# Kernel tuning notes

Hardware: AMD Instinct MI355X
Metric: run time of the kernel (lower is better)

Reference implementation:

```python
import jax, jax.numpy as jnp
import numpy as np

VOCAB = 780
HIDDEN = 256
DEPTH = 6
N_NODES = 65536
N_MESS = 131072
MAX_NEI = 5
N_TREES = 2048


def setup_inputs() -> dict:
    key = jax.random.key(0)
    ks = jax.random.split(key, 16)
    s = 0.05  # weight scale to avoid gate saturation
    return {
        "fnode": jax.random.randint(ks[0], (N_NODES,), 0, VOCAB),
        "fmess": jax.random.randint(ks[1], (N_MESS,), 0, N_NODES),
        "node_graph": jax.random.randint(ks[2], (N_NODES, MAX_NEI), 0, N_MESS),
        "mess_graph": jax.random.randint(ks[3], (N_MESS, MAX_NEI), 0, N_MESS),
        "scope_ids": jnp.sort(jax.random.randint(ks[4], (N_NODES,), 0, N_TREES)),
        "emb": jax.random.normal(ks[5], (VOCAB, HIDDEN), jnp.float32) * s,
        "Wz_w": jax.random.normal(ks[6], (2 * HIDDEN, HIDDEN), jnp.float32) * s,
        "Wz_b": jax.random.normal(ks[7], (HIDDEN,), jnp.float32) * s,
        "Wr_w": jax.random.normal(ks[8], (HIDDEN, HIDDEN), jnp.float32) * s,
        "Ur_w": jax.random.normal(ks[9], (HIDDEN, HIDDEN), jnp.float32) * s,
        "Ur_b": jax.random.normal(ks[10], (HIDDEN,), jnp.float32) * s,
        "Wh_w": jax.random.normal(ks[11], (2 * HIDDEN, HIDDEN), jnp.float32) * s,
        "Wh_b": jax.random.normal(ks[12], (HIDDEN,), jnp.float32) * s,
        "out_w": jax.random.normal(ks[13], (2 * HIDDEN, HIDDEN), jnp.float32) * s,
        "out_b": jax.random.normal(ks[14], (HIDDEN,), jnp.float32) * s,
    }


def reference(fnode, fmess, node_graph, mess_graph, scope_ids,
              emb, Wz_w, Wz_b, Wr_w, Ur_w, Ur_b, Wh_w, Wh_b, out_w, out_b):
    x_node = emb[fnode]            # [N, H] embedding lookup
    x = x_node[fmess]              # [M, H] source-node feature per message
    M = mess_graph.shape[0]
    mask = jnp.ones((M, 1), x.dtype).at[0].set(0.0)  # message 0 is padding
    r1 = x @ Wr_w                  # W_r(x), constant across depth (no bias)

    def gru_step(h, _):
        h_nei = h[mess_graph]                                  # [M, K, H] gather
        sum_h = h_nei.sum(axis=1)                              # [M, H]
        z = jax.nn.sigmoid(jnp.concatenate([x, sum_h], 1) @ Wz_w + Wz_b)
        r = jax.nn.sigmoid(r1[:, None, :] + h_nei @ Ur_w + Ur_b)  # [M, K, H]
        sum_gh = (r * h_nei).sum(axis=1)
        pre_h = jnp.tanh(jnp.concatenate([x, sum_gh], 1) @ Wh_w + Wh_b)
        h_new = ((1.0 - z) * sum_h + z * pre_h) * mask
        return h_new, None

    h0 = jnp.zeros((M, HIDDEN), x.dtype)
    h, _ = jax.lax.scan(gru_step, h0, None, length=DEPTH)

    mess_nei = h[node_graph].sum(axis=1)                       # [N, H]
    node_vec = jax.nn.relu(jnp.concatenate([x_node, mess_nei], 1) @ out_w + out_b)

    # per-tree mean over contiguous scopes (segment mean)
    sums = jax.ops.segment_sum(node_vec, scope_ids, num_segments=N_TREES)
    counts = jax.ops.segment_sum(jnp.ones((node_vec.shape[0],), node_vec.dtype),
                                 scope_ids, num_segments=N_TREES)
    return sums / jnp.maximum(counts, 1.0)[:, None]
```

## Files before the change

kernel.cpp:

```cpp
#include <hip/hip_runtime.h>


#define HD 256
#define NNODES 65536
#define NMESS 131072
#define NVOCAB 780
#define NTREES 2048
#define MAXNEI 5
#define BM 128
#define BMF 32
#define LDF 264

typedef short bfrag __attribute__((ext_vector_type(8)));
typedef short s16x8 __attribute__((ext_vector_type(8)));
typedef float f32x4v __attribute__((ext_vector_type(4)));
typedef unsigned short ush;

__device__ __forceinline__ float bf2f(ush u) {
    union { unsigned int u; float f; } v; v.u = ((unsigned int)u) << 16; return v.f;
}
__device__ __forceinline__ ush f2bf_fast(float f) {
    union { float f; unsigned int u; } v; v.f = f;
    return (ush)((v.u + 0x8000u) >> 16);
}
__device__ __forceinline__ unsigned int pack2bf(float hi, float lo) {
    union { float f; unsigned int u; } a, b; a.f = hi; b.f = lo;
    return __builtin_amdgcn_perm(a.u + 0x8000u, b.u + 0x8000u, 0x07060302u);
}
__device__ __forceinline__ float sigm(float x) {
    return __builtin_amdgcn_rcpf(1.f + __expf(-x));
}
__device__ __forceinline__ float tanh_fast(float x) {
    return 1.f - 2.f * __builtin_amdgcn_rcpf(__expf(2.f * x) + 1.f);
}
__device__ __forceinline__ void async16(const ush* g, ush* l) {
    __builtin_amdgcn_global_load_lds(
        (const __attribute__((address_space(1))) unsigned int*)(g),
        (__attribute__((address_space(3))) unsigned int*)(l), 16, 0, 0);
}

__global__ __launch_bounds__(256) void prep_tables_sk(
    const float* __restrict__ emb,
    const float* __restrict__ Wz_w, const float* __restrict__ Wz_b,
    const float* __restrict__ Wr_w, const float* __restrict__ Ur_b,
    const float* __restrict__ Wh_w, const float* __restrict__ Wh_b,
    const float* __restrict__ out_w, const float* __restrict__ out_b,
    float* __restrict__ embR, float* __restrict__ embZ,
    float* __restrict__ embH, float* __restrict__ embO)
{
    __shared__ __align__(16) float e[4][64];
    int t = threadIdx.x;
    int b0 = blockIdx.x * 4;
    int k0 = blockIdx.y * 64;
    e[t >> 6][t & 63] = emb[(b0 + (t >> 6)) * HD + k0 + (t & 63)];
    __syncthreads();
    float aR[4] = {0,0,0,0}, aZ[4] = {0,0,0,0}, aH[4] = {0,0,0,0}, aO[4] = {0,0,0,0};
    for (int kk = 0; kk < 64; kk++) {
        int k = k0 + kk;
        float wr = Wr_w[k * HD + t];
        float wz = Wz_w[k * HD + t];
        float wh = Wh_w[k * HD + t];
        float wo = out_w[k * HD + t];
        #pragma unroll
        for (int r = 0; r < 4; r++) {
            float ev = e[r][kk];
            aR[r] += ev * wr; aZ[r] += ev * wz; aH[r] += ev * wh; aO[r] += ev * wo;
        }
    }
    if (blockIdx.y == 0) {
        float br = Ur_b[t], bz = Wz_b[t], bh = Wh_b[t], bo = out_b[t];
        #pragma unroll
        for (int r = 0; r < 4; r++) { aR[r] += br; aZ[r] += bz; aH[r] += bh; aO[r] += bo; }
    }
    #pragma unroll
    for (int r = 0; r < 4; r++) {
        atomicAdd(&embR[(b0 + r) * HD + t], aR[r]);
        atomicAdd(&embZ[(b0 + r) * HD + t], aZ[r]);
        atomicAdd(&embH[(b0 + r) * HD + t], aH[r]);
        atomicAdd(&embO[(b0 + r) * HD + t], aO[r]);
    }
}

__global__ __launch_bounds__(256) void h1fill(
    const float* __restrict__ embZ, const float* __restrict__ embH,
    ush* __restrict__ h1tab)
{
    int i = blockIdx.x * HD + threadIdx.x;
    h1tab[i] = f2bf_fast(sigm(embZ[i]) * tanh_fast(embH[i]));
}

__global__ __launch_bounds__(256) void h1u_sk(
    const ush* __restrict__ h1tab, const float* __restrict__ Ur_w,
    float* __restrict__ embU)
{
    __shared__ __align__(16) float e[4][64];
    int t = threadIdx.x;
    int b0 = blockIdx.x * 4;
    int k0 = blockIdx.y * 64;
    e[t >> 6][t & 63] = bf2f(h1tab[(b0 + (t >> 6)) * HD + k0 + (t & 63)]);
    __syncthreads();
    float aU[4] = {0,0,0,0};
    for (int kk = 0; kk < 64; kk++) {
        float w = Ur_w[(k0 + kk) * HD + t];
        #pragma unroll
        for (int r = 0; r < 4; r++) aU[r] += e[r][kk] * w;
    }
    #pragma unroll
    for (int r = 0; r < 4; r++) atomicAdd(&embU[(b0 + r) * HD + t], aU[r]);
}

__global__ __launch_bounds__(256) void prep_wt(
    const float* __restrict__ Ur_w, const float* __restrict__ Wz_w,
    const float* __restrict__ Wh_w, const float* __restrict__ out_w,
    ush* __restrict__ UrT, ush* __restrict__ Wo2T,
    ush* __restrict__ Wz_p, ush* __restrict__ Wh_p)
{
    int idx = blockIdx.x * 256 + threadIdx.x;
    int n = idx >> 8, k = idx & 255;
    UrT[idx]  = f2bf_fast(Ur_w[k * HD + n]);
    Wo2T[idx] = f2bf_fast(out_w[(HD + k) * HD + n]);
    int paddr = ((((n >> 4) * 8 + (k >> 5)) * 64 + ((k >> 3) & 3) * 16 + (n & 15)) << 3) + (k & 7);
    Wz_p[paddr] = f2bf_fast(Wz_w[(HD + k) * HD + n]);
    Wh_p[paddr] = f2bf_fast(Wh_w[(HD + k) * HD + n]);
}

__global__ __launch_bounds__(256) void prep_vmess(
    const int* __restrict__ fnode, const int* __restrict__ fmess,
    int* __restrict__ v_mess)
{
    int m = blockIdx.x * 256 + threadIdx.x;
    v_mess[m] = fnode[fmess[m]];
}

__global__ __launch_bounds__(256) void fill_h1(
    const ush* __restrict__ h1tab, const float* __restrict__ embU,
    const int* __restrict__ v_mess,
    ush* __restrict__ h, ush* __restrict__ hU)
{
    int t = blockIdx.x * 256 + threadIdx.x;
    int m = t >> 5;
    int c = (t & 31) * 8;
    int v = v_mess[m];
    s16x8 o = *(const s16x8*)&h1tab[v * HD + c];
    float4 u0 = *(const float4*)&embU[v * HD + c];
    float4 u1 = *(const float4*)&embU[v * HD + c + 4];
    uint4 up;
    up.x = pack2bf(u0.y, u0.x); up.y = pack2bf(u0.w, u0.z);
    up.z = pack2bf(u1.y, u1.x); up.w = pack2bf(u1.w, u1.z);
    if (m == 0) { o = (s16x8){0,0,0,0,0,0,0,0}; up.x = up.y = up.z = up.w = 0; }
    *(s16x8*)&h[(size_t)m * HD + c] = o;
    *(uint4*)&hU[(size_t)m * HD + c] = up;
}

template<int MODE>
__global__ __launch_bounds__(512) void gemm_tile(
    const ush* __restrict__ A, const ush* __restrict__ Bt,
    void* __restrict__ C,
    const float* __restrict__ etab, const int* __restrict__ vids)
{
    __shared__ __align__(16) ush As[BM * 64];
    __shared__ __align__(16) ush Bs[HD * 64];
    int tid = threadIdx.x;
    int wave = tid >> 6, lane = tid & 63;
    int wm = wave >> 2, wn = wave & 3;
    int quad = lane >> 4, l16 = lane & 15;
    int row0 = blockIdx.x * BM;

    const ush* aG[2]; ush* aL[2];
    const ush* bG[4]; ush* bL[4];
    #pragma unroll
    for (int u = 0; u < 2; u++) {
        int cch = wave * 2 + u;
        int s = cch * 64 + lane;
        int r = s >> 3, p = s & 7, q = p ^ (r & 7);
        aG[u] = A + (size_t)(row0 + r) * HD + q * 8;
        aL[u] = &As[cch * 512];
    }
    #pragma unroll
    for (int u = 0; u < 4; u++) {
        int cch = wave * 4 + u;
        int s = cch * 64 + lane;
        int r = s >> 3, p = s & 7, q = p ^ (r & 7);
        bG[u] = Bt + (size_t)r * HD + q * 8;
        bL[u] = &Bs[cch * 512];
    }

    f32x4v acc[4][4] = {};

    for (int k0 = 0; k0 < HD; k0 += 64) {
        #pragma unroll
        for (int u = 0; u < 2; u++) async16(aG[u] + k0, aL[u]);
        #pragma unroll
        for (int u = 0; u < 4; u++) async16(bG[u] + k0, bL[u]);
        __syncthreads();
        #pragma unroll
        for (int ks = 0; ks < 64; ks += 32) {
            bfrag af[4], bff[4];
            #pragma unroll
            for (int i = 0; i < 4; i++) {
                int r = wm * 64 + i * 16 + l16;
                int q = (ks >> 3) + quad, p = q ^ (r & 7);
                af[i] = *(const bfrag*)&As[r * 64 + p * 8];
            }
            #pragma unroll
            for (int j = 0; j < 4; j++) {
                int r = wn * 64 + j * 16 + l16;
                int q = (ks >> 3) + quad, p = q ^ (r & 7);
                bff[j] = *(const bfrag*)&Bs[r * 64 + p * 8];
            }
            #pragma unroll
            for (int i = 0; i < 4; i++)
                #pragma unroll
                for (int j = 0; j < 4; j++)
                    acc[i][j] = __builtin_amdgcn_mfma_f32_16x16x32_bf16(af[i], bff[j], acc[i][j], 0, 0, 0);
        }
        __syncthreads();
    }
    #pragma unroll
    for (int i = 0; i < 4; i++) {
        #pragma unroll
        for (int j = 0; j < 4; j++) {
            int Cc = wn * 64 + j * 16 + l16;
            #pragma unroll
            for (int r = 0; r < 4; r++) {
                int Rr = row0 + wm * 64 + i * 16 + quad * 4 + r;
                float v = acc[i][j][r];
                if (MODE == 0) {
                    ((ush*)C)[(size_t)Rr * HD + Cc] = f2bf_fast(v);
                } else {
                    float o = v + etab[vids[Rr] * HD + Cc];
                    ((float*)C)[(size_t)Rr * HD + Cc] = fmaxf(o, 0.f);
                }
            }
        }
    }
}

__global__ __launch_bounds__(256, 4) void fused_step(
    const ush* __restrict__ h, const ush* __restrict__ hU,
    const int* __restrict__ mg, const int* __restrict__ v_mess,
    const float* __restrict__ embR, const float* __restrict__ embZ,
    const float* __restrict__ embH,
    const ush* __restrict__ Wz_p, const ush* __restrict__ Wh_p,
    ush* __restrict__ h_next)
{
    __shared__ __align__(16) ush sh[BMF * LDF];
    __shared__ __align__(16) ush sg[BMF * LDF];
    int tid = threadIdx.x;
    int wv = tid >> 6, lane = tid & 63;
    int quad = lane >> 4, l16 = lane & 15;
    int m0 = blockIdx.x * BMF;

    #pragma unroll 2
    for (int it = 0; it < 4; it++) {
        int g = it * 256 + tid;
        int ml = g >> 5;
        int c = (g & 31) * 8;
        int m = m0 + ml;
        int v = v_mess[m];
        float rb[8];
        *(float4*)&rb[0] = *(const float4*)&embR[v * HD + c];
        *(float4*)&rb[4] = *(const float4*)&embR[v * HD + c + 4];
        float ah[8] = {0,0,0,0,0,0,0,0};
        float ag[8] = {0,0,0,0,0,0,0,0};
        #pragma unroll
        for (int kn = 0; kn < MAXNEI; kn++) {
            int j = mg[m * MAXNEI + kn];
            s16x8 hv = *(const s16x8*)&h[(size_t)j * HD + c];
            s16x8 uv = *(const s16x8*)&hU[(size_t)j * HD + c];
            #pragma unroll
            for (int e = 0; e < 8; e++) {
                float hf = bf2f((ush)hv[e]);
                ah[e] += hf;
                ag[e] += sigm(rb[e] + bf2f((ush)uv[e])) * hf;
            }
        }
        uint4 oh, og;
        oh.x = pack2bf(ah[1], ah[0]); oh.y = pack2bf(ah[3], ah[2]);
        oh.z = pack2bf(ah[5], ah[4]); oh.w = pack2bf(ah[7], ah[6]);
        og.x = pack2bf(ag[1], ag[0]); og.y = pack2bf(ag[3], ag[2]);
        og.z = pack2bf(ag[5], ag[4]); og.w = pack2bf(ag[7], ag[6]);
        *(uint4*)&sh[ml * LDF + c] = oh;
        *(uint4*)&sg[ml * LDF + c] = og;
    }
    __syncthreads();

    f32x4v az[2][4] = {}, ap[2][4] = {};
    #pragma unroll
    for (int ksi = 0; ksi < 8; ksi++) {
        int ks = ksi * 32;
        bfrag ahf[2], agf[2], bz[4], bh[4];
        #pragma unroll
        for (int i = 0; i < 2; i++) {
            ahf[i] = *(const bfrag*)&sh[(i * 16 + l16) * LDF + ks + quad * 8];
            agf[i] = *(const bfrag*)&sg[(i * 16 + l16) * LDF + ks + quad * 8];
        }
        #pragma unroll
        for (int j = 0; j < 4; j++) {
            int f = ((wv * 4 + j) * 8 + ksi) * 64 + lane;
            bz[j] = *(const bfrag*)&Wz_p[(size_t)f * 8];
            bh[j] = *(const bfrag*)&Wh_p[(size_t)f * 8];
        }
        #pragma unroll
        for (int i = 0; i < 2; i++)
            #pragma unroll
            for (int j = 0; j < 4; j++) {
                az[i][j] = __builtin_amdgcn_mfma_f32_16x16x32_bf16(ahf[i], bz[j], az[i][j], 0, 0, 0);
                ap[i][j] = __builtin_amdgcn_mfma_f32_16x16x32_bf16(agf[i], bh[j], ap[i][j], 0, 0, 0);
            }
    }

    #pragma unroll
    for (int i = 0; i < 2; i++) {
        #pragma unroll
        for (int r = 0; r < 4; r++) {
            int rl = i * 16 + quad * 4 + r;
            int Rg = m0 + rl;
            int v = v_mess[Rg];
            #pragma unroll
            for (int j = 0; j < 4; j++) {
                int col = wv * 64 + j * 16 + l16;
                float z = sigm(az[i][j][r] + embZ[v * HD + col]);
                float pre = tanh_fast(ap[i][j][r] + embH[v * HD + col]);
                float shv = bf2f(sh[rl * LDF + col]);
                float hn = (1.f - z) * shv + z * pre;
                if (Rg == 0) hn = 0.f;
                h_next[(size_t)Rg * HD + col] = f2bf_fast(hn);
            }
        }
    }
}

__global__ __launch_bounds__(256) void gather_nodes(
    const ush* __restrict__ h, const int* __restrict__ ng,
    ush* __restrict__ mess_nei)
{
    int wave = threadIdx.x >> 6, lane = threadIdx.x & 63;
    int half = lane >> 5, li = lane & 31;
    int n = blockIdx.x * 8 + wave * 2 + half;
    int c = li * 8;
    float a[8] = {0,0,0,0,0,0,0,0};
    #pragma unroll
    for (int k = 0; k < MAXNEI; k++) {
        int j = ng[n * MAXNEI + k];
        s16x8 hv = *(const s16x8*)&h[(size_t)j * HD + c];
        #pragma unroll
        for (int e = 0; e < 8; e++) a[e] += bf2f((ush)hv[e]);
    }
    uint4 o;
    o.x = pack2bf(a[1], a[0]); o.y = pack2bf(a[3], a[2]);
    o.z = pack2bf(a[5], a[4]); o.w = pack2bf(a[7], a[6]);
    *(uint4*)&mess_nei[(size_t)n * HD + c] = o;
}

__device__ __forceinline__ int lower_bound_dev(const int* a, int n, int key) {
    int lo = 0, hi = n;
    while (lo < hi) { int mid = (lo + hi) >> 1; if (a[mid] < key) lo = mid + 1; else hi = mid; }
    return lo;
}

__global__ __launch_bounds__(256) void segment_mean(
    const float* __restrict__ node_vec, const int* __restrict__ scope,
    float* __restrict__ out)
{
    int t = blockIdx.x;
    int c = threadIdx.x;
    int lo = lower_bound_dev(scope, NNODES, t);
    int hi = lower_bound_dev(scope, NNODES, t + 1);
    float acc = 0.f;
    for (int n = lo; n < hi; n++) acc += node_vec[(size_t)n * HD + c];
    int cnt = hi - lo;
    out[t * HD + c] = cnt > 0 ? acc / (float)cnt : 0.f;
}

extern "C" void kernel_launch(void* const* d_in, const int* in_sizes, int n_in,
                              void* d_out, int out_size, void* d_ws, size_t ws_size,
                              hipStream_t stream)
{
    const int*   fnode      = (const int*)d_in[0];
    const int*   fmess      = (const int*)d_in[1];
    const int*   node_graph = (const int*)d_in[2];
    const int*   mess_graph = (const int*)d_in[3];
    const int*   scope_ids  = (const int*)d_in[4];
    const float* emb        = (const float*)d_in[5];
    const float* Wz_w       = (const float*)d_in[6];
    const float* Wz_b       = (const float*)d_in[7];
    const float* Wr_w       = (const float*)d_in[8];
    const float* Ur_w       = (const float*)d_in[9];
    const float* Ur_b       = (const float*)d_in[10];
    const float* Wh_w       = (const float*)d_in[11];
    const float* Wh_b       = (const float*)d_in[12];
    const float* out_w      = (const float*)d_in[13];
    const float* out_b      = (const float*)d_in[14];

    char* ws = (char*)d_ws;
    const size_t MHB = (size_t)NMESS * HD * 2;
    ush* P0 = (ush*)ws; ws += MHB;
    ush* P1 = (ush*)ws; ws += MHB;
    ush* PU = (ush*)ws; ws += MHB;
    float* embR = (float*)ws; ws += (size_t)NVOCAB * HD * 4;
    float* embZ = (float*)ws; ws += (size_t)NVOCAB * HD * 4;
    float* embH = (float*)ws; ws += (size_t)NVOCAB * HD * 4;
    float* embO = (float*)ws; ws += (size_t)NVOCAB * HD * 4;
    float* embU = (float*)ws; ws += (size_t)NVOCAB * HD * 4;
    ush* h1tab = (ush*)ws; ws += (size_t)NVOCAB * HD * 2;
    ush* UrT   = (ush*)ws; ws += (size_t)HD * HD * 2;
    ush* Wo2T  = (ush*)ws; ws += (size_t)HD * HD * 2;
    ush* Wz_p  = (ush*)ws; ws += (size_t)HD * HD * 2;
    ush* Wh_p  = (ush*)ws; ws += (size_t)HD * HD * 2;
    int* v_mess = (int*)ws; ws += (size_t)NMESS * 4;
    if ((size_t)(ws - (char*)d_ws) > ws_size) return;

    hipMemsetAsync(embR, 0, (size_t)5 * NVOCAB * HD * 4, stream);
    prep_tables_sk<<<dim3(NVOCAB / 4, 4), 256, 0, stream>>>(
        emb, Wz_w, Wz_b, Wr_w, Ur_b, Wh_w, Wh_b, out_w, out_b,
        embR, embZ, embH, embO);
    h1fill<<<NVOCAB, 256, 0, stream>>>(embZ, embH, h1tab);
    h1u_sk<<<dim3(NVOCAB / 4, 4), 256, 0, stream>>>(h1tab, Ur_w, embU);
    prep_wt<<<HD * HD / 256, 256, 0, stream>>>(Ur_w, Wz_w, Wh_w, out_w,
                                               UrT, Wo2T, Wz_p, Wh_p);
    prep_vmess<<<NMESS / 256, 256, 0, stream>>>(fnode, fmess, v_mess);
    fill_h1<<<NMESS * 32 / 256, 256, 0, stream>>>(h1tab, embU, v_mess, P0, PU);

    ush* hc = P0;
    ush* hn = P1;
    for (int d = 1; d < 6; d++) {
        if (d > 1)
            gemm_tile<0><<<NMESS / BM, 512, 0, stream>>>(hc, UrT, PU, nullptr, nullptr);
        fused_step<<<NMESS / BMF, 256, 0, stream>>>(hc, PU, mess_graph, v_mess,
                                                    embR, embZ, embH, Wz_p, Wh_p, hn);
        ush* tmp = hc; hc = hn; hn = tmp;
    }
    ush* mess_nei = PU;
    float* node_vec = (float*)hn;
    gather_nodes<<<NNODES / 8, 256, 0, stream>>>(hc, node_graph, mess_nei);
    gemm_tile<3><<<NNODES / BM, 512, 0, stream>>>(mess_nei, Wo2T, node_vec, embO, fnode);
    segment_mean<<<NTREES, 256, 0, stream>>>(node_vec, scope_ids, (float*)d_out);
}
```

Before: 1.190 ms.

## Fuse Ur GEMM into GRU step epilogue and store hU as fp8

Drops the separate per-depth gemm_tile that computed h@Ur. Each fused_step now stages its new h tile in LDS, writes it out coalesced, and runs the Ur MFMA on that tile in the epilogue. The product hU is stored as fp8 instead of bf16, which halves the bytes of the most-gathered neighbour stream. This removes one full read and write pass over the message matrix per depth, at the cost of fp8 rounding error inside the reset-gate sigmoid and extra work per step block.

```diff
diff --git a/kernel.cpp b/kernel.cpp
--- a/kernel.cpp
+++ b/kernel.cpp
@@ -14,10 +14,18 @@
 typedef short bfrag __attribute__((ext_vector_type(8)));
 typedef short s16x8 __attribute__((ext_vector_type(8)));
 typedef float f32x4v __attribute__((ext_vector_type(4)));
+typedef float f32x2 __attribute__((ext_vector_type(2)));
 typedef unsigned short ush;
+typedef unsigned char u8;
 
 __device__ __forceinline__ float bf2f(ush u) {
     union { unsigned int u; float f; } v; v.u = ((unsigned int)u) << 16; return v.f;
+}
+__device__ __forceinline__ float bfu_lo(unsigned int w) {
+    union { unsigned int u; float f; } v; v.u = w << 16; return v.f;
+}
+__device__ __forceinline__ float bfu_hi(unsigned int w) {
+    union { unsigned int u; float f; } v; v.u = w & 0xffff0000u; return v.f;
 }
 __device__ __forceinline__ ush f2bf_fast(float f) {
     union { float f; unsigned int u; } v; v.f = f;
@@ -37,6 +45,13 @@
     __builtin_amdgcn_global_load_lds(
         (const __attribute__((address_space(1))) unsigned int*)(g),
         (__attribute__((address_space(3))) unsigned int*)(l), 16, 0, 0);
+}
+__device__ __forceinline__ uint2 pack8fp8(const float* f) {
+    int lo = __builtin_amdgcn_cvt_pk_fp8_f32(f[0], f[1], 0, 0);
+    lo = __builtin_amdgcn_cvt_pk_fp8_f32(f[2], f[3], lo, 1);
+    int hi = __builtin_amdgcn_cvt_pk_fp8_f32(f[4], f[5], 0, 0);
+    hi = __builtin_amdgcn_cvt_pk_fp8_f32(f[6], f[7], hi, 1);
+    uint2 o; o.x = (unsigned int)lo; o.y = (unsigned int)hi; return o;
 }
 
 __global__ __launch_bounds__(256) void prep_tables_sk(
@@ -112,16 +127,16 @@
 __global__ __launch_bounds__(256) void prep_wt(
     const float* __restrict__ Ur_w, const float* __restrict__ Wz_w,
     const float* __restrict__ Wh_w, const float* __restrict__ out_w,
-    ush* __restrict__ UrT, ush* __restrict__ Wo2T,
-    ush* __restrict__ Wz_p, ush* __restrict__ Wh_p)
+    ush* __restrict__ Wo2T,
+    ush* __restrict__ Wz_p, ush* __restrict__ Wh_p, ush* __restrict__ Ur_p)
 {
     int idx = blockIdx.x * 256 + threadIdx.x;
     int n = idx >> 8, k = idx & 255;
-    UrT[idx]  = f2bf_fast(Ur_w[k * HD + n]);
     Wo2T[idx] = f2bf_fast(out_w[(HD + k) * HD + n]);
     int paddr = ((((n >> 4) * 8 + (k >> 5)) * 64 + ((k >> 3) & 3) * 16 + (n & 15)) << 3) + (k & 7);
     Wz_p[paddr] = f2bf_fast(Wz_w[(HD + k) * HD + n]);
     Wh_p[paddr] = f2bf_fast(Wh_w[(HD + k) * HD + n]);
+    Ur_p[paddr] = f2bf_fast(Ur_w[k * HD + n]);
 }
 
 __global__ __launch_bounds__(256) void prep_vmess(
@@ -135,27 +150,25 @@
 __global__ __launch_bounds__(256) void fill_h1(
     const ush* __restrict__ h1tab, const float* __restrict__ embU,
     const int* __restrict__ v_mess,
-    ush* __restrict__ h, ush* __restrict__ hU)
+    ush* __restrict__ h, u8* __restrict__ hU8)
 {
     int t = blockIdx.x * 256 + threadIdx.x;
     int m = t >> 5;
     int c = (t & 31) * 8;
     int v = v_mess[m];
     s16x8 o = *(const s16x8*)&h1tab[v * HD + c];
-    float4 u0 = *(const float4*)&embU[v * HD + c];
-    float4 u1 = *(const float4*)&embU[v * HD + c + 4];
-    uint4 up;
-    up.x = pack2bf(u0.y, u0.x); up.y = pack2bf(u0.w, u0.z);
-    up.z = pack2bf(u1.y, u1.x); up.w = pack2bf(u1.w, u1.z);
-    if (m == 0) { o = (s16x8){0,0,0,0,0,0,0,0}; up.x = up.y = up.z = up.w = 0; }
+    float u[8];
+    *(float4*)&u[0] = *(const float4*)&embU[v * HD + c];
+    *(float4*)&u[4] = *(const float4*)&embU[v * HD + c + 4];
+    uint2 up = pack8fp8(u);
+    if (m == 0) { o = (s16x8){0,0,0,0,0,0,0,0}; up.x = up.y = 0; }
     *(s16x8*)&h[(size_t)m * HD + c] = o;
-    *(uint4*)&hU[(size_t)m * HD + c] = up;
-}
-
-template<int MODE>
-__global__ __launch_bounds__(512) void gemm_tile(
+    *(uint2*)&hU8[(size_t)m * HD + c] = up;
+}
+
+__global__ __launch_bounds__(512) void gemm_out(
     const ush* __restrict__ A, const ush* __restrict__ Bt,
-    void* __restrict__ C,
+    float* __restrict__ C,
     const float* __restrict__ etab, const int* __restrict__ vids)
 {
     __shared__ __align__(16) ush As[BM * 64];
@@ -224,25 +237,22 @@
             #pragma unroll
             for (int r = 0; r < 4; r++) {
                 int Rr = row0 + wm * 64 + i * 16 + quad * 4 + r;
-                float v = acc[i][j][r];
-                if (MODE == 0) {
-                    ((ush*)C)[(size_t)Rr * HD + Cc] = f2bf_fast(v);
-                } else {
-                    float o = v + etab[vids[Rr] * HD + Cc];
-                    ((float*)C)[(size_t)Rr * HD + Cc] = fmaxf(o, 0.f);
-                }
-            }
-        }
-    }
-}
-
+                float o = acc[i][j][r] + etab[vids[Rr] * HD + Cc];
+                C[(size_t)Rr * HD + Cc] = fmaxf(o, 0.f);
+            }
+        }
+    }
+}
+
+template<int EMIT_HU>
 __global__ __launch_bounds__(256, 4) void fused_step(
-    const ush* __restrict__ h, const ush* __restrict__ hU,
+    const ush* __restrict__ h, const u8* __restrict__ hU8,
     const int* __restrict__ mg, const int* __restrict__ v_mess,
     const float* __restrict__ embR, const float* __restrict__ embZ,
     const float* __restrict__ embH,
     const ush* __restrict__ Wz_p, const ush* __restrict__ Wh_p,
-    ush* __restrict__ h_next)
+    const ush* __restrict__ Ur_p,
+    ush* __restrict__ h_next, u8* __restrict__ hU8_next)
 {
     __shared__ __align__(16) ush sh[BMF * LDF];
     __shared__ __align__(16) ush sg[BMF * LDF];
@@ -267,12 +277,17 @@
         for (int kn = 0; kn < MAXNEI; kn++) {
             int j = mg[m * MAXNEI + kn];
             s16x8 hv = *(const s16x8*)&h[(size_t)j * HD + c];
-            s16x8 uv = *(const s16x8*)&hU[(size_t)j * HD + c];
+            uint2 uv = *(const uint2*)&hU8[(size_t)j * HD + c];
+            f32x2 u01 = __builtin_amdgcn_cvt_pk_f32_fp8((int)uv.x, false);
+            f32x2 u23 = __builtin_amdgcn_cvt_pk_f32_fp8((int)uv.x, true);
+            f32x2 u45 = __builtin_amdgcn_cvt_pk_f32_fp8((int)uv.y, false);
+            f32x2 u67 = __builtin_amdgcn_cvt_pk_f32_fp8((int)uv.y, true);
+            float uf[8] = {u01.x, u01.y, u23.x, u23.y, u45.x, u45.y, u67.x, u67.y};
             #pragma unroll
             for (int e = 0; e < 8; e++) {
                 float hf = bf2f((ush)hv[e]);
                 ah[e] += hf;
-                ag[e] += sigm(rb[e] + bf2f((ush)uv[e])) * hf;
+                ag[e] += sigm(rb[e] + uf[e]) * hf;
             }
         }
         uint4 oh, og;
@@ -325,8 +340,70 @@
                 float shv = bf2f(sh[rl * LDF + col]);
                 float hn = (1.f - z) * shv + z * pre;
                 if (Rg == 0) hn = 0.f;
-                h_next[(size_t)Rg * HD + col] = f2bf_fast(hn);
-            }
+                az[i][j][r] = hn;
+            }
+        }
+    }
+    __syncthreads();
+
+    #pragma unroll
+    for (int i = 0; i < 2; i++)
+        #pragma unroll
+        for (int j = 0; j < 4; j++) {
+            int col = wv * 64 + j * 16 + l16;
+            #pragma unroll
+            for (int r = 0; r < 4; r++)
+                sg[(i * 16 + quad * 4 + r) * LDF + col] = f2bf_fast(az[i][j][r]);
+        }
+    __syncthreads();
+    #pragma unroll
+    for (int it = 0; it < 4; it++) {
+        int g = it * 256 + tid;
+        int ml = g >> 5;
+        int c = (g & 31) * 8;
+        *(uint4*)&h_next[(size_t)(m0 + ml) * HD + c] = *(const uint4*)&sg[ml * LDF + c];
+    }
+
+    if (EMIT_HU) {
+        f32x4v au[2][4] = {};
+        #pragma unroll
+        for (int ksi = 0; ksi < 8; ksi++) {
+            int ks = ksi * 32;
+            bfrag af[2], bu[4];
+            #pragma unroll
+            for (int i = 0; i < 2; i++)
+                af[i] = *(const bfrag*)&sg[(i * 16 + l16) * LDF + ks + quad * 8];
+            #pragma unroll
+            for (int j = 0; j < 4; j++) {
+                int f = ((wv * 4 + j) * 8 + ksi) * 64 + lane;
+                bu[j] = *(const bfrag*)&Ur_p[(size_t)f * 8];
+            }
+            #pragma unroll
+            for (int i = 0; i < 2; i++)
+                #pragma unroll
+                for (int j = 0; j < 4; j++)
+                    au[i][j] = __builtin_amdgcn_mfma_f32_16x16x32_bf16(af[i], bu[j], au[i][j], 0, 0, 0);
+        }
+        #pragma unroll
+        for (int i = 0; i < 2; i++)
+            #pragma unroll
+            for (int j = 0; j < 4; j++) {
+                int col = wv * 64 + j * 16 + l16;
+                #pragma unroll
+                for (int r = 0; r < 4; r++)
+                    sh[(i * 16 + quad * 4 + r) * LDF + col] = f2bf_fast(au[i][j][r]);
+            }
+        __syncthreads();
+        #pragma unroll
+        for (int it = 0; it < 4; it++) {
+            int g = it * 256 + tid;
+            int ml = g >> 5;
+            int c = (g & 31) * 8;
+            uint4 w = *(const uint4*)&sh[ml * LDF + c];
+            float f[8] = { bfu_lo(w.x), bfu_hi(w.x), bfu_lo(w.y), bfu_hi(w.y),
+                           bfu_lo(w.z), bfu_hi(w.z), bfu_lo(w.w), bfu_hi(w.w) };
+            uint2 o = pack8fp8(f);
+            *(uint2*)&hU8_next[(size_t)(m0 + ml) * HD + c] = o;
         }
     }
 }
@@ -395,19 +472,21 @@
 
     char* ws = (char*)d_ws;
     const size_t MHB = (size_t)NMESS * HD * 2;
+    const size_t MH8 = (size_t)NMESS * HD;
     ush* P0 = (ush*)ws; ws += MHB;
     ush* P1 = (ush*)ws; ws += MHB;
-    ush* PU = (ush*)ws; ws += MHB;
+    u8* U0 = (u8*)ws; ws += MH8;
+    u8* U1 = (u8*)ws; ws += MH8;
     float* embR = (float*)ws; ws += (size_t)NVOCAB * HD * 4;
     float* embZ = (float*)ws; ws += (size_t)NVOCAB * HD * 4;
     float* embH = (float*)ws; ws += (size_t)NVOCAB * HD * 4;
     float* embO = (float*)ws; ws += (size_t)NVOCAB * HD * 4;
     float* embU = (float*)ws; ws += (size_t)NVOCAB * HD * 4;
     ush* h1tab = (ush*)ws; ws += (size_t)NVOCAB * HD * 2;
-    ush* UrT   = (ush*)ws; ws += (size_t)HD * HD * 2;
     ush* Wo2T  = (ush*)ws; ws += (size_t)HD * HD * 2;
     ush* Wz_p  = (ush*)ws; ws += (size_t)HD * HD * 2;
     ush* Wh_p  = (ush*)ws; ws += (size_t)HD * HD * 2;
+    ush* Ur_p  = (ush*)ws; ws += (size_t)HD * HD * 2;
     int* v_mess = (int*)ws; ws += (size_t)NMESS * 4;
     if ((size_t)(ws - (char*)d_ws) > ws_size) return;
 
@@ -418,22 +497,27 @@
     h1fill<<<NVOCAB, 256, 0, stream>>>(embZ, embH, h1tab);
     h1u_sk<<<dim3(NVOCAB / 4, 4), 256, 0, stream>>>(h1tab, Ur_w, embU);
     prep_wt<<<HD * HD / 256, 256, 0, stream>>>(Ur_w, Wz_w, Wh_w, out_w,
-                                               UrT, Wo2T, Wz_p, Wh_p);
+                                               Wo2T, Wz_p, Wh_p, Ur_p);
     prep_vmess<<<NMESS / 256, 256, 0, stream>>>(fnode, fmess, v_mess);
-    fill_h1<<<NMESS * 32 / 256, 256, 0, stream>>>(h1tab, embU, v_mess, P0, PU);
-
-    ush* hc = P0;
-    ush* hn = P1;
-    for (int d = 1; d < 6; d++) {
-        if (d > 1)
-            gemm_tile<0><<<NMESS / BM, 512, 0, stream>>>(hc, UrT, PU, nullptr, nullptr);
-        fused_step<<<NMESS / BMF, 256, 0, stream>>>(hc, PU, mess_graph, v_mess,
-                                                    embR, embZ, embH, Wz_p, Wh_p, hn);
-        ush* tmp = hc; hc = hn; hn = tmp;
-    }
-    ush* mess_nei = PU;
-    float* node_vec = (float*)hn;
+    fill_h1<<<NMESS * 32 / 256, 256, 0, stream>>>(h1tab, embU, v_mess, P0, U0);
+
+    ush* hc = P0; ush* hn = P1;
+    u8* uc = U0; u8* un = U1;
+    for (int d = 1; d < 5; d++) {
+        fused_step<1><<<NMESS / BMF, 256, 0, stream>>>(hc, uc, mess_graph, v_mess,
+                                                       embR, embZ, embH,
+                                                       Wz_p, Wh_p, Ur_p, hn, un);
+        { ush* t = hc; hc = hn; hn = t; }
+        { u8* t = uc; uc = un; un = t; }
+    }
+    fused_step<0><<<NMESS / BMF, 256, 0, stream>>>(hc, uc, mess_graph, v_mess,
+                                                   embR, embZ, embH,
+                                                   Wz_p, Wh_p, Ur_p, hn, nullptr);
+    hc = hn;
+
+    ush* mess_nei = (ush*)U0;
+    float* node_vec = (float*)(hc == P0 ? P1 : P0);
     gather_nodes<<<NNODES / 8, 256, 0, stream>>>(hc, node_graph, mess_nei);
-    gemm_tile<3><<<NNODES / BM, 512, 0, stream>>>(mess_nei, Wo2T, node_vec, embO, fnode);
+    gemm_out<<<NNODES / BM, 512, 0, stream>>>(mess_nei, Wo2T, node_vec, embO, fnode);
     segment_mean<<<NTREES, 256, 0, stream>>>(node_vec, scope_ids, (float*)d_out);
 }
```

Result: faster. 1.087 ms (-8.7%).
